# Optimization experiments

Measured on AMD Instinct MI355X. Metric: run time of the kernel, lower is better.

Reference implementation:

```python
import jax, jax.numpy as jnp
import numpy as np

N_UE = 100000
N_AP = 10000
N_E = 1600000
D = 64
H = 128


def setup_inputs() -> dict:
    key = jax.random.key(0)
    ks = jax.random.split(key, 10)
    s = 0.05
    return {
        "ue_hid": jax.random.normal(ks[0], (N_UE, D), jnp.float32),
        "ap_hid": jax.random.normal(ks[1], (N_AP, D), jnp.float32),
        "edge_hid": jax.random.normal(ks[2], (N_E, D), jnp.float32),
        "src": jax.random.randint(ks[3], (N_E,), 0, N_UE),
        "dst": jax.random.randint(ks[4], (N_E,), 0, N_AP),
        "W1a": jax.random.normal(ks[5], (2 * D, H), jnp.float32) * s,
        "b1a": jnp.zeros((H,), jnp.float32),
        "W1b": jax.random.normal(ks[6], (H, H), jnp.float32) * s,
        "b1b": jnp.zeros((H,), jnp.float32),
        "W2a": jax.random.normal(ks[7], (D + H, H), jnp.float32) * s,
        "b2a": jnp.zeros((H,), jnp.float32),
        "W2b": jax.random.normal(ks[8], (H, D), jnp.float32) * s,
        "b2b": jnp.zeros((D,), jnp.float32),
    }


def reference(ue_hid, ap_hid, edge_hid, src, dst,
              W1a, b1a, W1b, b1b, W2a, b2a, W2b, b2b):
    # message: concat(edge_feature, src UE feature) -> [E, 2D]
    msg = jnp.concatenate([edge_hid, ue_hid[src]], axis=-1)
    # mlp1 applied per edge (DGL applies it inside reduce on the mailbox,
    # which is equivalent to per-edge application followed by segment sum)
    h = jnp.maximum(msg @ W1a + b1a, 0.0) @ W1b + b1b          # [E, H]
    # sum over mailbox (all edges with the same destination AP)
    agg = jax.ops.segment_sum(h, dst, num_segments=N_AP)        # [N_AP, H]
    # mlp2 on concat(AP hid, aggregated messages)
    z = jnp.concatenate([ap_hid, agg], axis=-1)                 # [N_AP, D+H]
    new_ap = jnp.maximum(z @ W2a + b2a, 0.0) @ W2b + b2b        # [N_AP, D]
    return new_ap
```

## Files before the change

kernel.cpp:

```cpp
#include <hip/hip_runtime.h>

#define N_UE 100000
#define N_AP 10000
#define N_E  1600000
#define NTILE (N_E / 128)

typedef float f32x4 __attribute__((ext_vector_type(4)));
typedef int   i32x2 __attribute__((ext_vector_type(2)));
typedef short s8b   __attribute__((ext_vector_type(8)));
typedef short s4b   __attribute__((ext_vector_type(4)));

static __device__ __forceinline__ unsigned short f2bf(float x) {
  union { float f; unsigned int u; } v; v.f = x;
  unsigned int r = v.u + 0x7fffu + ((v.u >> 16) & 1u);
  return (unsigned short)(r >> 16);
}

__global__ void apk0_prep(const float* __restrict__ W1a, short* __restrict__ WTg,
                          int* __restrict__ counts, float* __restrict__ aggW) {
  int i = blockIdx.x * 256 + threadIdx.x, n = gridDim.x * 256;
  for (int x = i; x < 128 * 128; x += n) {
    int col = x >> 7, k = x & 127;
    WTg[x] = (short)f2bf(W1a[k * 128 + col]);
  }
  for (int x = i; x < N_AP; x += n) counts[x] = 0;
  for (int x = i; x < N_AP * 128 / 4; x += n)
    ((f32x4*)aggW)[x] = (f32x4){0.f, 0.f, 0.f, 0.f};
}

__global__ void apk2_hist(const int* __restrict__ dst, int* __restrict__ counts) {
  int i = blockIdx.x * blockDim.x + threadIdx.x;
  int stride = gridDim.x * blockDim.x;
  for (; i < N_E; i += stride) atomicAdd(&counts[dst[i]], 1);
}

__global__ __launch_bounds__(256) void apk3a_scanlocal(
    const int* __restrict__ counts, int* __restrict__ offsets,
    int* __restrict__ bsum) {
  __shared__ int p[256];
  int t = threadIdx.x, idx = blockIdx.x * 256 + t;
  int v = (idx < N_AP) ? counts[idx] : 0;
  p[t] = v;
  __syncthreads();
  for (int d = 1; d < 256; d <<= 1) {
    int s2 = p[t] + ((t >= d) ? p[t - d] : 0);
    __syncthreads();
    p[t] = s2;
    __syncthreads();
  }
  if (idx < N_AP) offsets[idx] = p[t] - v;
  if (t == 255) bsum[blockIdx.x] = p[255];
}

__global__ __launch_bounds__(256) void apk3b_scanbase(
    int* __restrict__ offsets, const int* __restrict__ bsum) {
  __shared__ int base;
  int t = threadIdx.x, idx = blockIdx.x * 256 + t;
  if (t == 0) {
    int b = 0;
    for (int k = 0; k < (int)blockIdx.x; k++) b += bsum[k];
    base = b;
  }
  __syncthreads();
  if (idx < N_AP) offsets[idx] += base;
}

__global__ void apk4_scatter(const int* __restrict__ dst, const int* __restrict__ src,
                             int* __restrict__ offsets, i32x2* __restrict__ pair) {
  int i = blockIdx.x * blockDim.x + threadIdx.x;
  int stride = gridDim.x * blockDim.x;
  for (; i < N_E; i += stride) {
    int d = dst[i], s = src[i];
    int pos = atomicAdd(&offsets[d], 1);
    i32x2 v;
    v[0] = i | ((d & 0x7FF) << 21);
    v[1] = s | ((d >> 11) << 17);
    pair[pos] = v;
  }
}

__global__ __launch_bounds__(256, 4) void apk5_edges(
    const float* __restrict__ edge_hid, const float* __restrict__ ue_hid,
    const short* __restrict__ WTg, const float* __restrict__ b1a,
    const i32x2* __restrict__ pair, float* __restrict__ aggW) {
  __shared__ short A[128][132];
  __shared__ int segs[128];
  __shared__ int eix[128];
  __shared__ int six[128];
  int t = threadIdx.x;
  int wave = t >> 6, lane = t & 63, quad = lane >> 4, l16 = lane & 15;

  s8b bf[2][4];
  for (int ct = 0; ct < 2; ct++)
    for (int ks = 0; ks < 4; ks++)
      bf[ct][ks] = *(const s8b*)&WTg[(wave * 32 + ct * 16 + l16) * 128 +
                                     ks * 32 + quad * 8];
  float bias0 = b1a[wave * 32 + l16];
  float bias1 = b1a[wave * 32 + 16 + l16];

  int runseg = -1;
  float run0 = 0.f, run1 = 0.f;
  auto flush = [&]() {
    if (runseg >= 0) {
      float f0 = run0 + __shfl_xor(run0, 16); f0 += __shfl_xor(f0, 32);
      float f1 = run1 + __shfl_xor(run1, 16); f1 += __shfl_xor(f1, 32);
      if (quad == 0) {
        atomicAdd(&aggW[(size_t)runseg * 128 + wave * 32 + l16], f0);
        atomicAdd(&aggW[(size_t)runseg * 128 + wave * 32 + 16 + l16], f1);
      }
    }
  };

  const int r8 = t >> 5, half = (t >> 4) & 1, chunk = t & 15;
  for (int tile = blockIdx.x; tile < NTILE; tile += gridDim.x) {
    __syncthreads();
    if (t < 128) {
      i32x2 tr = pair[(size_t)tile * 128 + t];
      segs[t] = (int)((unsigned)tr[0] >> 21) | (((tr[1] >> 17) & 7) << 11);
      eix[t] = tr[0] & 0x1FFFFF;
      six[t] = tr[1] & 0x1FFFF;
    }
    __syncthreads();
    {
      const float* bases[16];
      #pragma unroll
      for (int it = 0; it < 16; it++) {
        int row = it * 8 + r8;
        bases[it] = half ? (ue_hid + (size_t)six[row] * 64)
                         : (edge_hid + (size_t)eix[row] * 64);
      }
      #pragma unroll
      for (int it = 0; it < 16; it++) {
        int row = it * 8 + r8;
        f32x4 v = ((const f32x4*)bases[it])[chunk];
        s4b pk;
        pk[0] = (short)f2bf(v[0]); pk[1] = (short)f2bf(v[1]);
        pk[2] = (short)f2bf(v[2]); pk[3] = (short)f2bf(v[3]);
        *(s4b*)&A[row][half * 64 + chunk * 4] = pk;
      }
    }
    __syncthreads();

    for (int rt = 0; rt < 8; rt++) {
      s8b a0 = *(const s8b*)&A[rt * 16 + l16][0 + quad * 8];
      s8b a1 = *(const s8b*)&A[rt * 16 + l16][32 + quad * 8];
      s8b a2 = *(const s8b*)&A[rt * 16 + l16][64 + quad * 8];
      s8b a3 = *(const s8b*)&A[rt * 16 + l16][96 + quad * 8];
      f32x4 c0 = {0.f, 0.f, 0.f, 0.f}, c1 = {0.f, 0.f, 0.f, 0.f};
      c0 = __builtin_amdgcn_mfma_f32_16x16x32_bf16(a0, bf[0][0], c0, 0, 0, 0);
      c0 = __builtin_amdgcn_mfma_f32_16x16x32_bf16(a1, bf[0][1], c0, 0, 0, 0);
      c0 = __builtin_amdgcn_mfma_f32_16x16x32_bf16(a2, bf[0][2], c0, 0, 0, 0);
      c0 = __builtin_amdgcn_mfma_f32_16x16x32_bf16(a3, bf[0][3], c0, 0, 0, 0);
      c1 = __builtin_amdgcn_mfma_f32_16x16x32_bf16(a0, bf[1][0], c1, 0, 0, 0);
      c1 = __builtin_amdgcn_mfma_f32_16x16x32_bf16(a1, bf[1][1], c1, 0, 0, 0);
      c1 = __builtin_amdgcn_mfma_f32_16x16x32_bf16(a2, bf[1][2], c1, 0, 0, 0);
      c1 = __builtin_amdgcn_mfma_f32_16x16x32_bf16(a3, bf[1][3], c1, 0, 0, 0);
      float t0[4], t1[4];
      #pragma unroll
      for (int j = 0; j < 4; j++) {
        t0[j] = fmaxf(c0[j] + bias0, 0.f);
        t1[j] = fmaxf(c1[j] + bias1, 0.f);
      }
      int gb = rt * 16;
      int sF = segs[gb], sL = segs[gb + 15];
      if (sF == sL) {
        if (sF != runseg) { flush(); runseg = sF; run0 = 0.f; run1 = 0.f; }
        run0 += t0[0] + t0[1] + t0[2] + t0[3];
        run1 += t1[0] + t1[1] + t1[2] + t1[3];
      } else {
        int sj[4];
        #pragma unroll
        for (int j = 0; j < 4; j++) sj[j] = segs[gb + quad * 4 + j];
        for (int sg = sF; sg <= sL; sg++) {
          float v0 = 0.f, v1 = 0.f;
          #pragma unroll
          for (int j = 0; j < 4; j++)
            if (sj[j] == sg) { v0 += t0[j]; v1 += t1[j]; }
          if (sg == runseg) { run0 += v0; run1 += v1; }
          else { flush(); runseg = sg; run0 = v0; run1 = v1; }
        }
      }
    }
  }
  flush();
}

__global__ __launch_bounds__(256) void apk6_mlp2(
    const float* __restrict__ ap_hid, const float* __restrict__ W1b,
    const float* __restrict__ b1b, const float* __restrict__ W2a,
    const float* __restrict__ b2a, const float* __restrict__ W2b,
    const float* __restrict__ b2b, const float* __restrict__ aggW,
    const int* __restrict__ counts, float* __restrict__ out) {
  __shared__ float wbuf[64 * 128];
  __shared__ float zrows[16 * 128];
  __shared__ float yrows[16 * 128];
  __shared__ float arows[16 * 64];
  __shared__ float cbuf[16];
  int t = threadIdx.x;
  int apb = blockIdx.x * 16;
  for (int i = t; i < 16 * 128 / 4; i += 256)
    ((float4*)zrows)[i] = ((const float4*)(aggW + (size_t)apb * 128))[i];
  for (int i = t; i < 16 * 64 / 4; i += 256)
    ((float4*)arows)[i] = ((const float4*)(ap_hid + (size_t)apb * 64))[i];
  if (t < 16) cbuf[t] = (float)counts[apb + t];
  int j = t & 127, half = t >> 7;
  {
    float bb = b1b[j];
    __syncthreads();
    float acc[8];
    for (int r = 0; r < 8; r++) acc[r] = cbuf[half * 8 + r] * bb;
    for (int pp = 0; pp < 2; pp++) {
      __syncthreads();
      for (int i = t; i < 64 * 128 / 4; i += 256)
        ((float4*)wbuf)[i] = ((const float4*)(W1b + pp * 64 * 128))[i];
      __syncthreads();
      for (int k = 0; k < 64; k++) {
        float w = wbuf[k * 128 + j];
        for (int r = 0; r < 8; r++)
          acc[r] += zrows[(half * 8 + r) * 128 + (pp * 64 + k)] * w;
      }
    }
    for (int r = 0; r < 8; r++) yrows[(half * 8 + r) * 128 + j] = acc[r];
  }
  {
    float acc2[8];
    float bb = b2a[j];
    for (int r = 0; r < 8; r++) acc2[r] = bb;
    __syncthreads();
    for (int i = t; i < 64 * 128 / 4; i += 256)
      ((float4*)wbuf)[i] = ((const float4*)W2a)[i];
    __syncthreads();
    for (int k = 0; k < 64; k++) {
      float w = wbuf[k * 128 + j];
      for (int r = 0; r < 8; r++) acc2[r] += arows[(half * 8 + r) * 64 + k] * w;
    }
    for (int pp = 0; pp < 2; pp++) {
      __syncthreads();
      for (int i = t; i < 64 * 128 / 4; i += 256)
        ((float4*)wbuf)[i] = ((const float4*)(W2a + (64 + pp * 64) * 128))[i];
      __syncthreads();
      for (int k = 0; k < 64; k++) {
        float w = wbuf[k * 128 + j];
        for (int r = 0; r < 8; r++)
          acc2[r] += yrows[(half * 8 + r) * 128 + (pp * 64 + k)] * w;
      }
    }
    __syncthreads();
    for (int r = 0; r < 8; r++)
      zrows[(half * 8 + r) * 128 + j] = fmaxf(acc2[r], 0.f);
  }
  {
    __syncthreads();
    for (int i = t; i < 128 * 64 / 4; i += 256)
      ((float4*)wbuf)[i] = ((const float4*)W2b)[i];
    __syncthreads();
    int i2 = t & 63, q = t >> 6;
    float acc3[4];
    float bb = b2b[i2];
    for (int r = 0; r < 4; r++) acc3[r] = bb;
    for (int k = 0; k < 128; k++) {
      float w = wbuf[k * 64 + i2];
      for (int r = 0; r < 4; r++) acc3[r] += zrows[(q * 4 + r) * 128 + k] * w;
    }
    for (int r = 0; r < 4; r++)
      out[(size_t)(apb + q * 4 + r) * 64 + i2] = acc3[r];
  }
}

extern "C" void kernel_launch(void* const* d_in, const int* in_sizes, int n_in,
                              void* d_out, int out_size, void* d_ws, size_t ws_size,
                              hipStream_t stream) {
  const float* ue_hid   = (const float*)d_in[0];
  const float* ap_hid   = (const float*)d_in[1];
  const float* edge_hid = (const float*)d_in[2];
  const int*   src      = (const int*)d_in[3];
  const int*   dst      = (const int*)d_in[4];
  const float* W1a      = (const float*)d_in[5];
  const float* b1a      = (const float*)d_in[6];
  const float* W1b      = (const float*)d_in[7];
  const float* b1b      = (const float*)d_in[8];
  const float* W2a      = (const float*)d_in[9];
  const float* b2a      = (const float*)d_in[10];
  const float* W2b      = (const float*)d_in[11];
  const float* b2b      = (const float*)d_in[12];
  float* out = (float*)d_out;

  unsigned char* ws = (unsigned char*)d_ws;
  short* WTg    = (short*)(ws);
  int* counts   = (int*)(ws + 32768);
  int* offsets  = (int*)(ws + 73728);
  int* bsum     = (int*)(ws + 114688);
  float* aggW   = (float*)(ws + 118784);
  i32x2* pair   = (i32x2*)(ws + 5238784);

  apk0_prep<<<640, 256, 0, stream>>>(W1a, WTg, counts, aggW);
  apk2_hist<<<2048, 256, 0, stream>>>(dst, counts);
  apk3a_scanlocal<<<40, 256, 0, stream>>>(counts, offsets, bsum);
  apk3b_scanbase<<<40, 256, 0, stream>>>(offsets, bsum);
  apk4_scatter<<<2048, 256, 0, stream>>>(dst, src, offsets, pair);
  apk5_edges<<<2048, 256, 0, stream>>>(edge_hid, ue_hid, WTg, b1a, pair, aggW);
  apk6_mlp2<<<N_AP / 16, 256, 0, stream>>>(ap_hid, W1b, b1b, W2a, b2a, W2b, b2b,
                                           aggW, counts, out);
}
```

Measured before the change: 829.0 us.

## Software-pipeline edge gathers in register staging and vectorize index loads

The edge kernel now prefetches the next tile's gathered edge and UE rows into registers (16 f32x4 per thread) while the current tile runs its MFMA compute. The segment and index arrays in shared memory are double-buffered, and the pair loads are issued two tiles ahead. Histogram and scatter now read dst and src as int4, and their grids shrink to 1600 blocks. The extra staging registers force occupancy down from 4 to 3 blocks per CU, which could offset the latency hiding.

```diff
diff --git a/kernel.cpp b/kernel.cpp
--- a/kernel.cpp
+++ b/kernel.cpp
@@ -29,9 +29,15 @@
 }
 
 __global__ void apk2_hist(const int* __restrict__ dst, int* __restrict__ counts) {
-  int i = blockIdx.x * blockDim.x + threadIdx.x;
-  int stride = gridDim.x * blockDim.x;
-  for (; i < N_E; i += stride) atomicAdd(&counts[dst[i]], 1);
+  int i = blockIdx.x * 256 + threadIdx.x;
+  int n = gridDim.x * 256;
+  for (int x = i; x < N_E / 4; x += n) {
+    int4 d = ((const int4*)dst)[x];
+    atomicAdd(&counts[d.x], 1);
+    atomicAdd(&counts[d.y], 1);
+    atomicAdd(&counts[d.z], 1);
+    atomicAdd(&counts[d.w], 1);
+  }
 }
 
 __global__ __launch_bounds__(256) void apk3a_scanlocal(
@@ -67,26 +73,33 @@
 
 __global__ void apk4_scatter(const int* __restrict__ dst, const int* __restrict__ src,
                              int* __restrict__ offsets, i32x2* __restrict__ pair) {
-  int i = blockIdx.x * blockDim.x + threadIdx.x;
-  int stride = gridDim.x * blockDim.x;
-  for (; i < N_E; i += stride) {
-    int d = dst[i], s = src[i];
-    int pos = atomicAdd(&offsets[d], 1);
-    i32x2 v;
-    v[0] = i | ((d & 0x7FF) << 21);
-    v[1] = s | ((d >> 11) << 17);
-    pair[pos] = v;
-  }
-}
-
-__global__ __launch_bounds__(256, 4) void apk5_edges(
+  int i = blockIdx.x * 256 + threadIdx.x;
+  int n = gridDim.x * 256;
+  for (int x = i; x < N_E / 4; x += n) {
+    int4 d = ((const int4*)dst)[x];
+    int4 s = ((const int4*)src)[x];
+    int e = x * 4;
+    int dd[4] = {d.x, d.y, d.z, d.w};
+    int ss[4] = {s.x, s.y, s.z, s.w};
+    #pragma unroll
+    for (int j = 0; j < 4; j++) {
+      int pos = atomicAdd(&offsets[dd[j]], 1);
+      i32x2 v;
+      v[0] = (e + j) | ((dd[j] & 0x7FF) << 21);
+      v[1] = ss[j] | ((dd[j] >> 11) << 17);
+      pair[pos] = v;
+    }
+  }
+}
+
+__global__ __launch_bounds__(256, 3) void apk5_edges(
     const float* __restrict__ edge_hid, const float* __restrict__ ue_hid,
     const short* __restrict__ WTg, const float* __restrict__ b1a,
     const i32x2* __restrict__ pair, float* __restrict__ aggW) {
   __shared__ short A[128][132];
-  __shared__ int segs[128];
-  __shared__ int eix[128];
-  __shared__ int six[128];
+  __shared__ int segs[2][128];
+  __shared__ int eix[2][128];
+  __shared__ int six[2][128];
   int t = threadIdx.x;
   int wave = t >> 6, lane = t & 63, quad = lane >> 4, l16 = lane & 15;
 
@@ -111,36 +124,61 @@
     }
   };
 
+  const int G = gridDim.x;
   const int r8 = t >> 5, half = (t >> 4) & 1, chunk = t & 15;
-  for (int tile = blockIdx.x; tile < NTILE; tile += gridDim.x) {
-    __syncthreads();
-    if (t < 128) {
-      i32x2 tr = pair[(size_t)tile * 128 + t];
-      segs[t] = (int)((unsigned)tr[0] >> 21) | (((tr[1] >> 17) & 7) << 11);
-      eix[t] = tr[0] & 0x1FFFFF;
-      six[t] = tr[1] & 0x1FFFF;
-    }
-    __syncthreads();
-    {
-      const float* bases[16];
+  const int T0 = blockIdx.x;
+
+  f32x4 stg[16];
+  i32x2 pr;
+
+  if (t < 128) {
+    i32x2 tr = pair[(size_t)T0 * 128 + t];
+    segs[0][t] = (int)((unsigned)tr[0] >> 21) | (((tr[1] >> 17) & 7) << 11);
+    eix[0][t] = tr[0] & 0x1FFFFF;
+    six[0][t] = tr[1] & 0x1FFFF;
+  }
+  __syncthreads();
+  if ((T0 + G) < NTILE && t < 128) pr = pair[(size_t)(T0 + G) * 128 + t];
+  #pragma unroll
+  for (int it = 0; it < 16; it++) {
+    int row = it * 8 + r8;
+    const float* base = half ? (ue_hid + (size_t)six[0][row] * 64)
+                             : (edge_hid + (size_t)eix[0][row] * 64);
+    stg[it] = ((const f32x4*)base)[chunk];
+  }
+
+  int cur = 0;
+  for (int T = T0; T < NTILE; T += G) {
+    int nxt = cur ^ 1;
+    bool hn  = (T + G) < NTILE;
+    bool hn2 = (T + 2 * G) < NTILE;
+    __syncthreads();
+    #pragma unroll
+    for (int it = 0; it < 16; it++) {
+      int row = it * 8 + r8;
+      f32x4 v = stg[it];
+      s4b pk;
+      pk[0] = (short)f2bf(v[0]); pk[1] = (short)f2bf(v[1]);
+      pk[2] = (short)f2bf(v[2]); pk[3] = (short)f2bf(v[3]);
+      *(s4b*)&A[row][half * 64 + chunk * 4] = pk;
+    }
+    if (hn && t < 128) {
+      segs[nxt][t] = (int)((unsigned)pr[0] >> 21) | (((pr[1] >> 17) & 7) << 11);
+      eix[nxt][t] = pr[0] & 0x1FFFFF;
+      six[nxt][t] = pr[1] & 0x1FFFF;
+    }
+    __syncthreads();
+    if (hn2 && t < 128) pr = pair[(size_t)(T + 2 * G) * 128 + t];
+    if (hn) {
       #pragma unroll
       for (int it = 0; it < 16; it++) {
         int row = it * 8 + r8;
-        bases[it] = half ? (ue_hid + (size_t)six[row] * 64)
-                         : (edge_hid + (size_t)eix[row] * 64);
-      }
-      #pragma unroll
-      for (int it = 0; it < 16; it++) {
-        int row = it * 8 + r8;
-        f32x4 v = ((const f32x4*)bases[it])[chunk];
-        s4b pk;
-        pk[0] = (short)f2bf(v[0]); pk[1] = (short)f2bf(v[1]);
-        pk[2] = (short)f2bf(v[2]); pk[3] = (short)f2bf(v[3]);
-        *(s4b*)&A[row][half * 64 + chunk * 4] = pk;
-      }
-    }
-    __syncthreads();
-
+        const float* base = half ? (ue_hid + (size_t)six[nxt][row] * 64)
+                                 : (edge_hid + (size_t)eix[nxt][row] * 64);
+        stg[it] = ((const f32x4*)base)[chunk];
+      }
+    }
+    const int* sg = segs[cur];
     for (int rt = 0; rt < 8; rt++) {
       s8b a0 = *(const s8b*)&A[rt * 16 + l16][0 + quad * 8];
       s8b a1 = *(const s8b*)&A[rt * 16 + l16][32 + quad * 8];
@@ -162,7 +200,7 @@
         t1[j] = fmaxf(c1[j] + bias1, 0.f);
       }
       int gb = rt * 16;
-      int sF = segs[gb], sL = segs[gb + 15];
+      int sF = sg[gb], sL = sg[gb + 15];
       if (sF == sL) {
         if (sF != runseg) { flush(); runseg = sF; run0 = 0.f; run1 = 0.f; }
         run0 += t0[0] + t0[1] + t0[2] + t0[3];
@@ -170,17 +208,18 @@
       } else {
         int sj[4];
         #pragma unroll
-        for (int j = 0; j < 4; j++) sj[j] = segs[gb + quad * 4 + j];
-        for (int sg = sF; sg <= sL; sg++) {
+        for (int j = 0; j < 4; j++) sj[j] = sg[gb + quad * 4 + j];
+        for (int sgv = sF; sgv <= sL; sgv++) {
           float v0 = 0.f, v1 = 0.f;
           #pragma unroll
           for (int j = 0; j < 4; j++)
-            if (sj[j] == sg) { v0 += t0[j]; v1 += t1[j]; }
-          if (sg == runseg) { run0 += v0; run1 += v1; }
-          else { flush(); runseg = sg; run0 = v0; run1 = v1; }
+            if (sj[j] == sgv) { v0 += t0[j]; v1 += t1[j]; }
+          if (sgv == runseg) { run0 += v0; run1 += v1; }
+          else { flush(); runseg = sgv; run0 = v0; run1 = v1; }
         }
       }
     }
+    cur = nxt;
   }
   flush();
 }
@@ -294,10 +333,10 @@
   i32x2* pair   = (i32x2*)(ws + 5238784);
 
   apk0_prep<<<640, 256, 0, stream>>>(W1a, WTg, counts, aggW);
-  apk2_hist<<<2048, 256, 0, stream>>>(dst, counts);
+  apk2_hist<<<1600, 256, 0, stream>>>(dst, counts);
   apk3a_scanlocal<<<40, 256, 0, stream>>>(counts, offsets, bsum);
   apk3b_scanbase<<<40, 256, 0, stream>>>(offsets, bsum);
-  apk4_scatter<<<2048, 256, 0, stream>>>(dst, src, offsets, pair);
+  apk4_scatter<<<1600, 256, 0, stream>>>(dst, src, offsets, pair);
   apk5_edges<<<2048, 256, 0, stream>>>(edge_hid, ue_hid, WTg, b1a, pair, aggW);
   apk6_mlp2<<<N_AP / 16, 256, 0, stream>>>(ap_hid, W1b, b1b, W2a, b2a, W2b, b2b,
                                            aggW, counts, out);
```

Measured after the change: 839.7 us. Within noise of the previous version (+1.3%).
